# Kernel tuning notes

Hardware: AMD Instinct MI355X
Metric: run time of the kernel (lower is better)

The kernel has to match this reference:

```python
import jax, jax.numpy as jnp
import numpy as np

H = 768
L = 9
M = 5            # max_span_length
CTX_RATIO = 0.5
NEG_INF = -1e30


def setup_inputs() -> dict:
    key = jax.random.key(0)
    ks = jax.random.split(key, 12)
    B, S = 4, 2048
    sc = 1.0 / np.sqrt(H)
    return {
        "sequence_output": jax.random.normal(ks[0], (B, S, H), dtype=jnp.float32),
        "Wc": jax.random.normal(ks[1], (H, L), dtype=jnp.float32) * sc,
        "bc": jnp.zeros((L,), dtype=jnp.float32),
        "wa": jax.random.normal(ks[2], (H,), dtype=jnp.float32) * sc,
        "ba": jnp.zeros((), dtype=jnp.float32),
        "W1": jax.random.normal(ks[3], (2 * H, H), dtype=jnp.float32) * (1.0 / np.sqrt(2 * H)),
        "b1": jnp.zeros((H,), dtype=jnp.float32),
        "gamma": jnp.ones((H,), dtype=jnp.float32),
        "beta": jnp.zeros((H,), dtype=jnp.float32),
        "W2": jax.random.normal(ks[4], (H, L), dtype=jnp.float32) * sc,
        "b2": jnp.zeros((L,), dtype=jnp.float32),
    }


def reference(sequence_output, Wc, bc, wa, ba, W1, b1, gamma, beta, W2, b2):
    x = sequence_output                        # [B,S,H]
    B, S, _ = x.shape
    base_logits = jnp.einsum('bsh,hl->bsl', x, Wc) + bc   # [B,S,L]

    # sliding-window indices: window [i-M, i+M] clipped to [0, S)
    offsets = jnp.arange(-M, M + 1)            # [W]
    idx = jnp.arange(S)[:, None] + offsets     # [S,W]
    valid = (idx >= 0) & (idx < S)             # [S,W]
    idx_c = jnp.clip(idx, 0, S - 1)            # [S,W]

    # attention scores over window (span_attention linear -> scalar per token)
    scores = jnp.einsum('bsh,h->bs', x, wa) + ba           # [B,S]
    win_scores = scores[:, idx_c]                          # [B,S,W]
    win_scores = jnp.where(valid[None], win_scores, NEG_INF)
    attn = jax.nn.softmax(win_scores, axis=-1)             # [B,S,W]

    win_tokens = x[:, idx_c]                               # [B,S,W,H] gather
    weighted_ctx = jnp.einsum('bsw,bswh->bsh', attn, win_tokens)

    token_with_ctx = jnp.concatenate([x, weighted_ctx], axis=-1)  # [B,S,2H]
    h = jnp.einsum('bsd,dh->bsh', token_with_ctx, W1) + b1
    # LayerNorm (eps = 1e-5, torch default)
    mu = jnp.mean(h, axis=-1, keepdims=True)
    var = jnp.mean((h - mu) ** 2, axis=-1, keepdims=True)
    h = (h - mu) * jax.lax.rsqrt(var + 1e-5) * gamma + beta
    h = jax.nn.gelu(h, approximate=False)                  # torch nn.GELU default (erf)
    ctx_logits = jnp.einsum('bsh,hl->bsl', h, W2) + b2

    return (1.0 - CTX_RATIO) * base_logits + CTX_RATIO * ctx_logits
```

## Files before the change

### kernel.cpp

```cpp
#include <hip/hip_runtime.h>
#include <hip/hip_bf16.h>
#include <math.h>

#define S_LEN 2048
#define BATCH 4
#define HDIM 768
#define LOUT 9
#define NROWS (BATCH*S_LEN)
#define K2H 1536
#define KHALF 768
#define WIN 11
#define NEG_INF_F (-1e30f)

typedef __attribute__((ext_vector_type(4))) float f32x4;
typedef __attribute__((ext_vector_type(8))) short bf16x8;

static __device__ __forceinline__ void async_ld16(const void* g, void* l) {
  __builtin_amdgcn_global_load_lds((const __attribute__((address_space(1))) void*)g,
                                   (__attribute__((address_space(3))) void*)l, 16, 0, 0);
}

static __device__ __forceinline__ unsigned short f2bf(float f) {
  union { float f; unsigned int u; } v; v.f = f;
  unsigned int u = v.u;
  unsigned int r = (u + 0x7fffu + ((u >> 16) & 1u)) >> 16;
  return (unsigned short)r;
}

static __device__ __forceinline__ float bf2f(unsigned short h) {
  union { unsigned int u; float f; } v; v.u = ((unsigned int)h) << 16;
  return v.f;
}

__global__ __launch_bounds__(256) void k_prep(const float* __restrict__ W1,
                                              unsigned short* __restrict__ W1t,
                                              const float* __restrict__ x,
                                              const float* __restrict__ wa,
                                              const float* __restrict__ ba,
                                              const float* __restrict__ Wc,
                                              const float* __restrict__ bc,
                                              unsigned short* __restrict__ xc,
                                              float* __restrict__ scores,
                                              float* __restrict__ base) {
  __shared__ float tile[32][33];
  if (blockIdx.x < 1152) {
    int bk = blockIdx.x % 48;
    int bn = blockIdx.x / 48;
    int tc = threadIdx.x % 32;
    int tr = threadIdx.x / 32;
    #pragma unroll
    for (int i = 0; i < 32; i += 8) {
      tile[tr + i][tc] = W1[(bk*32 + tr + i) * HDIM + bn*32 + tc];
    }
    __syncthreads();
    #pragma unroll
    for (int i = 0; i < 32; i += 8) {
      W1t[(bn*32 + tr + i) * K2H + bk*32 + tc] = f2bf(tile[tc][tr + i]);
    }
    return;
  }
  int bid = blockIdx.x - 1152;
  int lane = threadIdx.x & 63, wave = threadIdx.x >> 6;
  int row = bid * 4 + wave;
  const float* xr = x + (long)row * HDIM + lane * 12;
  float xv[12];
  { const float4 a = *(const float4*)(xr);
    const float4 b4 = *(const float4*)(xr + 4);
    const float4 c4 = *(const float4*)(xr + 8);
    xv[0]=a.x; xv[1]=a.y; xv[2]=a.z; xv[3]=a.w;
    xv[4]=b4.x; xv[5]=b4.y; xv[6]=b4.z; xv[7]=b4.w;
    xv[8]=c4.x; xv[9]=c4.y; xv[10]=c4.z; xv[11]=c4.w; }
  unsigned short* dst = xc + (long)row * K2H + lane * 12;
  #pragma unroll
  for (int q = 0; q < 3; ++q) {
    ushort4 o;
    o.x = f2bf(xv[q*4+0]); o.y = f2bf(xv[q*4+1]);
    o.z = f2bf(xv[q*4+2]); o.w = f2bf(xv[q*4+3]);
    *(ushort4*)(dst + q*4) = o;
  }
  const float* war = wa + lane * 12;
  float sc = 0.f;
  #pragma unroll
  for (int q = 0; q < 3; ++q) {
    const float4 w4 = *(const float4*)(war + q*4);
    sc += xv[q*4+0]*w4.x + xv[q*4+1]*w4.y + xv[q*4+2]*w4.z + xv[q*4+3]*w4.w;
  }
  const float* wcr = Wc + (long)lane * 12 * LOUT;
  float p[LOUT] = {};
  #pragma unroll
  for (int j = 0; j < 12; ++j) {
    const float xj = xv[j];
    #pragma unroll
    for (int l = 0; l < LOUT; ++l) p[l] += xj * wcr[j * LOUT + l];
  }
  #pragma unroll
  for (int m = 1; m < 64; m <<= 1) {
    sc += __shfl_xor(sc, m);
    #pragma unroll
    for (int l = 0; l < LOUT; ++l) p[l] += __shfl_xor(p[l], m);
  }
  if (lane == 0) {
    scores[row] = sc + ba[0];
    #pragma unroll
    for (int l = 0; l < LOUT; ++l) base[row * LOUT + l] = p[l] + bc[l];
  }
}

__global__ __launch_bounds__(256) void k_ctx(const float* __restrict__ scores,
                                             unsigned short* __restrict__ xc) {
  int lane = threadIdx.x & 63, wave = threadIdx.x >> 6;
  int row = blockIdx.x * 4 + wave;
  int b = row >> 11, s = row & 2047;
  float sw[WIN];
  int jcs[WIN];
  #pragma unroll
  for (int w = 0; w < WIN; ++w) {
    int j = s - 5 + w;
    bool valid = (j >= 0) && (j < S_LEN);
    int jc = valid ? j : (j < 0 ? 0 : S_LEN - 1);
    jcs[w] = b * S_LEN + jc;
    sw[w] = valid ? scores[b * S_LEN + jc] : NEG_INF_F;
  }
  float mx = sw[0];
  #pragma unroll
  for (int w = 1; w < WIN; ++w) mx = fmaxf(mx, sw[w]);
  float es[WIN], ssum = 0.f;
  #pragma unroll
  for (int w = 0; w < WIN; ++w) {
    es[w] = (sw[w] > -1e29f) ? __expf(sw[w] - mx) : 0.f;
    ssum += es[w];
  }
  float inv = 1.f / ssum;
  float c[12] = {};
  #pragma unroll
  for (int w = 0; w < WIN; ++w) {
    float aw = es[w] * inv;
    const unsigned short* src = xc + (long)jcs[w] * K2H + lane * 12;
    #pragma unroll
    for (int q = 0; q < 3; ++q) {
      const ushort4 uv = *(const ushort4*)(src + q*4);
      c[q*4+0] += aw * bf2f(uv.x);
      c[q*4+1] += aw * bf2f(uv.y);
      c[q*4+2] += aw * bf2f(uv.z);
      c[q*4+3] += aw * bf2f(uv.w);
    }
  }
  unsigned short* dst = xc + (long)row * K2H + HDIM + lane * 12;
  #pragma unroll
  for (int q = 0; q < 3; ++q) {
    ushort4 o;
    o.x = f2bf(c[q*4+0]); o.y = f2bf(c[q*4+1]);
    o.z = f2bf(c[q*4+2]); o.w = f2bf(c[q*4+3]);
    *(ushort4*)(dst + q*4) = o;
  }
}

__global__ __launch_bounds__(256, 3) void k_gemm(const unsigned short* __restrict__ A,
                                                 const unsigned short* __restrict__ Bt,
                                                 unsigned short* __restrict__ Hout) {
  __shared__ unsigned short As[2][128 * 32];
  __shared__ unsigned short Bs[2][128 * 32];
  int bid = blockIdx.x;
  int obid = (bid & 7) * 96 + (bid >> 3);
  int kh = obid / 384;
  int mt = obid % 384;
  int bm = mt / 6, bn = mt % 6;
  int t = threadIdx.x;
  int lane = t & 63, wave = t >> 6;
  int wm = wave >> 1, wn = wave & 1;

  int rowc = lane >> 2;
  int fST = ((lane >> 2) ^ (lane >> 4)) & 3;
  int sST = (lane & 3) ^ fST;
  const unsigned short* gA0 = A  + (long)(bm * 128 + wave * 16 + rowc) * K2H + kh * KHALF + sST * 8;
  const unsigned short* gB0 = Bt + (long)(bn * 128 + wave * 16 + rowc) * K2H + kh * KHALF + sST * 8;

  int fR = ((lane & 3) ^ ((lane >> 2) & 3)) & 3;
  int slR = ((lane >> 4) ^ fR) & 3;
  int arow = wm * 64 + (lane & 15);
  int brow = wn * 64 + (lane & 15);

  f32x4 acc[4][4] = {};

#define STAGE(buf, kt) do {                                                    \
    async_ld16(gA0 + (kt),            &As[buf][(wave * 16) * 32]);             \
    async_ld16(gA0 + 64 * K2H + (kt), &As[buf][(64 + wave * 16) * 32]);        \
    async_ld16(gB0 + (kt),            &Bs[buf][(wave * 16) * 32]);             \
    async_ld16(gB0 + 64 * K2H + (kt), &Bs[buf][(64 + wave * 16) * 32]);        \
  } while (0)

#define COMPUTE(buf) do {                                                      \
    bf16x8 af[4], bfv[4];                                                      \
    _Pragma("unroll")                                                          \
    for (int m = 0; m < 4; ++m)                                                \
      af[m] = *(const bf16x8*)(&As[buf][(arow + m * 16) * 32 + slR * 8]);      \
    _Pragma("unroll")                                                          \
    for (int n = 0; n < 4; ++n)                                                \
      bfv[n] = *(const bf16x8*)(&Bs[buf][(brow + n * 16) * 32 + slR * 8]);     \
    _Pragma("unroll")                                                          \
    for (int m = 0; m < 4; ++m)                                                \
      _Pragma("unroll")                                                        \
      for (int n = 0; n < 4; ++n)                                              \
        acc[m][n] = __builtin_amdgcn_mfma_f32_16x16x32_bf16(af[m], bfv[n], acc[m][n], 0, 0, 0); \
  } while (0)

  STAGE(0, 0);
  __syncthreads();
  int cur = 0;
  #pragma unroll 1
  for (int tt = 0; tt < 23; ++tt) {
    STAGE(cur ^ 1, (tt + 1) * 32);
    COMPUTE(cur);
    __syncthreads();
    cur ^= 1;
  }
  COMPUTE(cur);

  unsigned short* Hp = Hout + (long)kh * NROWS * HDIM;
  int orow = bm * 128 + wm * 64 + (lane >> 4) * 4;
  int ocol = bn * 128 + wn * 64 + (lane & 15);
  #pragma unroll
  for (int m = 0; m < 4; ++m)
    #pragma unroll
    for (int n = 0; n < 4; ++n) {
      int col = ocol + n * 16;
      #pragma unroll
      for (int r = 0; r < 4; ++r) {
        Hp[(long)(orow + m * 16 + r) * HDIM + col] = f2bf(acc[m][n][r]);
      }
    }
#undef STAGE
#undef COMPUTE
}

__global__ __launch_bounds__(256) void k_ln(const unsigned short* __restrict__ H0,
                                            const unsigned short* __restrict__ H1,
                                            const float* __restrict__ b1,
                                            const float* __restrict__ gamma,
                                            const float* __restrict__ beta,
                                            const float* __restrict__ W2,
                                            const float* __restrict__ b2,
                                            const float* __restrict__ base,
                                            float* __restrict__ out) {
  int lane = threadIdx.x & 63, wave = threadIdx.x >> 6;
  int row = blockIdx.x * 4 + wave;
  const unsigned short* h0p = H0 + (long)row * HDIM + lane * 12;
  const unsigned short* h1p = H1 + (long)row * HDIM + lane * 12;
  const float* b1p = b1 + lane * 12;
  float vv[12];
  #pragma unroll
  for (int q = 0; q < 3; ++q) {
    const ushort4 a = *(const ushort4*)(h0p + q*4);
    const ushort4 b4 = *(const ushort4*)(h1p + q*4);
    const float4 bb = *(const float4*)(b1p + q*4);
    vv[q*4+0] = bf2f(a.x) + bf2f(b4.x) + bb.x;
    vv[q*4+1] = bf2f(a.y) + bf2f(b4.y) + bb.y;
    vv[q*4+2] = bf2f(a.z) + bf2f(b4.z) + bb.z;
    vv[q*4+3] = bf2f(a.w) + bf2f(b4.w) + bb.w;
  }
  float s1 = 0.f, s2 = 0.f;
  #pragma unroll
  for (int j = 0; j < 12; ++j) { s1 += vv[j]; s2 += vv[j] * vv[j]; }
  #pragma unroll
  for (int m = 1; m < 64; m <<= 1) { s1 += __shfl_xor(s1, m); s2 += __shfl_xor(s2, m); }
  float mu = s1 * (1.f / HDIM);
  float var = s2 * (1.f / HDIM) - mu * mu;
  float rstd = rsqrtf(var + 1e-5f);
  const float* gp = gamma + lane * 12;
  const float* bp = beta + lane * 12;
  const float* w2r = W2 + (long)lane * 12 * LOUT;
  float p[LOUT] = {};
  #pragma unroll
  for (int q = 0; q < 3; ++q) {
    const float4 g4 = *(const float4*)(gp + q*4);
    const float4 be4 = *(const float4*)(bp + q*4);
    const float gv[4] = { g4.x, g4.y, g4.z, g4.w };
    const float bvv[4] = { be4.x, be4.y, be4.z, be4.w };
    #pragma unroll
    for (int k = 0; k < 4; ++k) {
      int j = q*4 + k;
      float g = (vv[j] - mu) * rstd * gv[k] + bvv[k];
      float gg = 0.5f * g * (1.f + erff(g * 0.70710678118654752f));
      #pragma unroll
      for (int l = 0; l < LOUT; ++l) p[l] += gg * w2r[j * LOUT + l];
    }
  }
  #pragma unroll
  for (int m = 1; m < 64; m <<= 1)
    #pragma unroll
    for (int l = 0; l < LOUT; ++l) p[l] += __shfl_xor(p[l], m);
  if (lane == 0) {
    #pragma unroll
    for (int l = 0; l < LOUT; ++l) {
      out[row * LOUT + l] = 0.5f * base[row * LOUT + l] + 0.5f * (p[l] + b2[l]);
    }
  }
}

extern "C" void kernel_launch(void* const* d_in, const int* in_sizes, int n_in,
                              void* d_out, int out_size, void* d_ws, size_t ws_size,
                              hipStream_t stream) {
  const float* x     = (const float*)d_in[0];
  const float* Wc    = (const float*)d_in[1];
  const float* bc    = (const float*)d_in[2];
  const float* wa    = (const float*)d_in[3];
  const float* ba    = (const float*)d_in[4];
  const float* W1    = (const float*)d_in[5];
  const float* b1    = (const float*)d_in[6];
  const float* gamma = (const float*)d_in[7];
  const float* beta  = (const float*)d_in[8];
  const float* W2    = (const float*)d_in[9];
  const float* b2    = (const float*)d_in[10];
  float* out = (float*)d_out;

  char* ws = (char*)d_ws;
  unsigned short* xc   = (unsigned short*)(ws);
  unsigned short* w1t  = (unsigned short*)(ws + 25165824);
  float* scores        = (float*)(ws + 27525120);
  float* base          = (float*)(ws + 27557888);
  unsigned short* hbuf = (unsigned short*)(ws + 27852800);

  k_prep <<<dim3(1152 + 2048), dim3(256), 0, stream>>>(W1, w1t, x, wa, ba, Wc, bc,
                                                       xc, scores, base);
  k_ctx  <<<dim3(2048), dim3(256), 0, stream>>>(scores, xc);
  k_gemm <<<dim3(768),  dim3(256), 0, stream>>>(xc, w1t, hbuf);
  k_ln   <<<dim3(2048), dim3(256), 0, stream>>>(hbuf, hbuf + (long)NROWS * HDIM, b1,
                                                gamma, beta, W2, b2, base, out);
}
```

Baseline: 171.0 us.

## Fuse four kernels into one persistent kernel with grid barriers

Merges the prep, context, GEMM and LayerNorm kernels into one persistent kernel of 768 blocks. The stages are separated by atomic-counter grid barriers, and the counter is reset by a memset before each launch. The aim is to remove the launch overhead and the gaps between kernels. In exchange it depends on all 768 blocks being resident at once (3 per CU is assumed), otherwise the barrier deadlocks. The elementwise stages now loop over rows with fewer waves and lose some occupancy.

```diff
diff --git a/kernel.cpp b/kernel.cpp
--- a/kernel.cpp
+++ b/kernel.cpp
@@ -11,6 +11,8 @@
 #define KHALF 768
 #define WIN 11
 #define NEG_INF_F (-1e30f)
+#define NBLK 768
+#define NWAVE (NBLK*4)
 
 typedef __attribute__((ext_vector_type(4))) float f32x4;
 typedef __attribute__((ext_vector_type(8))) short bf16x8;
@@ -32,155 +34,170 @@
   return v.f;
 }
 
-__global__ __launch_bounds__(256) void k_prep(const float* __restrict__ W1,
-                                              unsigned short* __restrict__ W1t,
-                                              const float* __restrict__ x,
-                                              const float* __restrict__ wa,
-                                              const float* __restrict__ ba,
-                                              const float* __restrict__ Wc,
-                                              const float* __restrict__ bc,
-                                              unsigned short* __restrict__ xc,
-                                              float* __restrict__ scores,
-                                              float* __restrict__ base) {
+static __device__ __forceinline__ void gridbar(unsigned* cnt, unsigned k) {
+  __syncthreads();
+  if (threadIdx.x == 0) {
+    __threadfence();
+    atomicAdd(cnt, 1u);
+    while (atomicAdd(cnt, 0u) < NBLK * k) __builtin_amdgcn_s_sleep(4);
+    __threadfence();
+  }
+  __syncthreads();
+}
+
+__global__ __launch_bounds__(256, 3)
+void k_fused(const float* __restrict__ x,
+             const float* __restrict__ Wc,
+             const float* __restrict__ bc,
+             const float* __restrict__ wa,
+             const float* __restrict__ ba,
+             const float* __restrict__ W1,
+             const float* __restrict__ b1,
+             const float* __restrict__ gamma,
+             const float* __restrict__ beta,
+             const float* __restrict__ W2,
+             const float* __restrict__ b2,
+             unsigned short* __restrict__ xc,
+             unsigned short* __restrict__ w1t,
+             float* __restrict__ scores,
+             float* __restrict__ base,
+             unsigned short* __restrict__ hbuf,
+             unsigned* __restrict__ barcnt,
+             float* __restrict__ out) {
   __shared__ float tile[32][33];
-  if (blockIdx.x < 1152) {
-    int bk = blockIdx.x % 48;
-    int bn = blockIdx.x / 48;
-    int tc = threadIdx.x % 32;
-    int tr = threadIdx.x / 32;
-    #pragma unroll
-    for (int i = 0; i < 32; i += 8) {
-      tile[tr + i][tc] = W1[(bk*32 + tr + i) * HDIM + bn*32 + tc];
-    }
-    __syncthreads();
-    #pragma unroll
-    for (int i = 0; i < 32; i += 8) {
-      W1t[(bn*32 + tr + i) * K2H + bk*32 + tc] = f2bf(tile[tc][tr + i]);
-    }
-    return;
-  }
-  int bid = blockIdx.x - 1152;
-  int lane = threadIdx.x & 63, wave = threadIdx.x >> 6;
-  int row = bid * 4 + wave;
-  const float* xr = x + (long)row * HDIM + lane * 12;
-  float xv[12];
-  { const float4 a = *(const float4*)(xr);
-    const float4 b4 = *(const float4*)(xr + 4);
-    const float4 c4 = *(const float4*)(xr + 8);
-    xv[0]=a.x; xv[1]=a.y; xv[2]=a.z; xv[3]=a.w;
-    xv[4]=b4.x; xv[5]=b4.y; xv[6]=b4.z; xv[7]=b4.w;
-    xv[8]=c4.x; xv[9]=c4.y; xv[10]=c4.z; xv[11]=c4.w; }
-  unsigned short* dst = xc + (long)row * K2H + lane * 12;
-  #pragma unroll
-  for (int q = 0; q < 3; ++q) {
-    ushort4 o;
-    o.x = f2bf(xv[q*4+0]); o.y = f2bf(xv[q*4+1]);
-    o.z = f2bf(xv[q*4+2]); o.w = f2bf(xv[q*4+3]);
-    *(ushort4*)(dst + q*4) = o;
-  }
-  const float* war = wa + lane * 12;
-  float sc = 0.f;
-  #pragma unroll
-  for (int q = 0; q < 3; ++q) {
-    const float4 w4 = *(const float4*)(war + q*4);
-    sc += xv[q*4+0]*w4.x + xv[q*4+1]*w4.y + xv[q*4+2]*w4.z + xv[q*4+3]*w4.w;
-  }
-  const float* wcr = Wc + (long)lane * 12 * LOUT;
-  float p[LOUT] = {};
-  #pragma unroll
-  for (int j = 0; j < 12; ++j) {
-    const float xj = xv[j];
-    #pragma unroll
-    for (int l = 0; l < LOUT; ++l) p[l] += xj * wcr[j * LOUT + l];
-  }
-  #pragma unroll
-  for (int m = 1; m < 64; m <<= 1) {
-    sc += __shfl_xor(sc, m);
-    #pragma unroll
-    for (int l = 0; l < LOUT; ++l) p[l] += __shfl_xor(p[l], m);
-  }
-  if (lane == 0) {
-    scores[row] = sc + ba[0];
-    #pragma unroll
-    for (int l = 0; l < LOUT; ++l) base[row * LOUT + l] = p[l] + bc[l];
-  }
-}
-
-__global__ __launch_bounds__(256) void k_ctx(const float* __restrict__ scores,
-                                             unsigned short* __restrict__ xc) {
-  int lane = threadIdx.x & 63, wave = threadIdx.x >> 6;
-  int row = blockIdx.x * 4 + wave;
-  int b = row >> 11, s = row & 2047;
-  float sw[WIN];
-  int jcs[WIN];
-  #pragma unroll
-  for (int w = 0; w < WIN; ++w) {
-    int j = s - 5 + w;
-    bool valid = (j >= 0) && (j < S_LEN);
-    int jc = valid ? j : (j < 0 ? 0 : S_LEN - 1);
-    jcs[w] = b * S_LEN + jc;
-    sw[w] = valid ? scores[b * S_LEN + jc] : NEG_INF_F;
-  }
-  float mx = sw[0];
-  #pragma unroll
-  for (int w = 1; w < WIN; ++w) mx = fmaxf(mx, sw[w]);
-  float es[WIN], ssum = 0.f;
-  #pragma unroll
-  for (int w = 0; w < WIN; ++w) {
-    es[w] = (sw[w] > -1e29f) ? __expf(sw[w] - mx) : 0.f;
-    ssum += es[w];
-  }
-  float inv = 1.f / ssum;
-  float c[12] = {};
-  #pragma unroll
-  for (int w = 0; w < WIN; ++w) {
-    float aw = es[w] * inv;
-    const unsigned short* src = xc + (long)jcs[w] * K2H + lane * 12;
-    #pragma unroll
-    for (int q = 0; q < 3; ++q) {
-      const ushort4 uv = *(const ushort4*)(src + q*4);
-      c[q*4+0] += aw * bf2f(uv.x);
-      c[q*4+1] += aw * bf2f(uv.y);
-      c[q*4+2] += aw * bf2f(uv.z);
-      c[q*4+3] += aw * bf2f(uv.w);
-    }
-  }
-  unsigned short* dst = xc + (long)row * K2H + HDIM + lane * 12;
-  #pragma unroll
-  for (int q = 0; q < 3; ++q) {
-    ushort4 o;
-    o.x = f2bf(c[q*4+0]); o.y = f2bf(c[q*4+1]);
-    o.z = f2bf(c[q*4+2]); o.w = f2bf(c[q*4+3]);
-    *(ushort4*)(dst + q*4) = o;
-  }
-}
-
-__global__ __launch_bounds__(256, 3) void k_gemm(const unsigned short* __restrict__ A,
-                                                 const unsigned short* __restrict__ Bt,
-                                                 unsigned short* __restrict__ Hout) {
   __shared__ unsigned short As[2][128 * 32];
   __shared__ unsigned short Bs[2][128 * 32];
-  int bid = blockIdx.x;
-  int obid = (bid & 7) * 96 + (bid >> 3);
-  int kh = obid / 384;
-  int mt = obid % 384;
-  int bm = mt / 6, bn = mt % 6;
-  int t = threadIdx.x;
-  int lane = t & 63, wave = t >> 6;
-  int wm = wave >> 1, wn = wave & 1;
-
-  int rowc = lane >> 2;
-  int fST = ((lane >> 2) ^ (lane >> 4)) & 3;
-  int sST = (lane & 3) ^ fST;
-  const unsigned short* gA0 = A  + (long)(bm * 128 + wave * 16 + rowc) * K2H + kh * KHALF + sST * 8;
-  const unsigned short* gB0 = Bt + (long)(bn * 128 + wave * 16 + rowc) * K2H + kh * KHALF + sST * 8;
-
-  int fR = ((lane & 3) ^ ((lane >> 2) & 3)) & 3;
-  int slR = ((lane >> 4) ^ fR) & 3;
-  int arow = wm * 64 + (lane & 15);
-  int brow = wn * 64 + (lane & 15);
-
-  f32x4 acc[4][4] = {};
+  int lane = threadIdx.x & 63, wave = threadIdx.x >> 6;
+  int gwid = blockIdx.x * 4 + wave;
+
+  for (int j = blockIdx.x; j < 1152; j += NBLK) {
+    int bk = j % 48, bn = j / 48;
+    int tc = threadIdx.x % 32, tr = threadIdx.x / 32;
+    #pragma unroll
+    for (int i = 0; i < 32; i += 8)
+      tile[tr + i][tc] = W1[(bk*32 + tr + i) * HDIM + bn*32 + tc];
+    __syncthreads();
+    #pragma unroll
+    for (int i = 0; i < 32; i += 8)
+      w1t[(bn*32 + tr + i) * K2H + bk*32 + tc] = f2bf(tile[tc][tr + i]);
+    __syncthreads();
+  }
+
+  for (int row = gwid; row < NROWS; row += NWAVE) {
+    const float* xr = x + (long)row * HDIM + lane * 12;
+    float xv[12];
+    { const float4 a = *(const float4*)(xr);
+      const float4 b4 = *(const float4*)(xr + 4);
+      const float4 c4 = *(const float4*)(xr + 8);
+      xv[0]=a.x; xv[1]=a.y; xv[2]=a.z; xv[3]=a.w;
+      xv[4]=b4.x; xv[5]=b4.y; xv[6]=b4.z; xv[7]=b4.w;
+      xv[8]=c4.x; xv[9]=c4.y; xv[10]=c4.z; xv[11]=c4.w; }
+    unsigned short* dst = xc + (long)row * K2H + lane * 12;
+    #pragma unroll
+    for (int q = 0; q < 3; ++q) {
+      ushort4 o;
+      o.x = f2bf(xv[q*4+0]); o.y = f2bf(xv[q*4+1]);
+      o.z = f2bf(xv[q*4+2]); o.w = f2bf(xv[q*4+3]);
+      *(ushort4*)(dst + q*4) = o;
+    }
+    const float* war = wa + lane * 12;
+    float sc = 0.f;
+    #pragma unroll
+    for (int q = 0; q < 3; ++q) {
+      const float4 w4 = *(const float4*)(war + q*4);
+      sc += xv[q*4+0]*w4.x + xv[q*4+1]*w4.y + xv[q*4+2]*w4.z + xv[q*4+3]*w4.w;
+    }
+    const float* wcr = Wc + (long)lane * 12 * LOUT;
+    float p[LOUT] = {};
+    #pragma unroll
+    for (int j = 0; j < 12; ++j) {
+      const float xj = xv[j];
+      #pragma unroll
+      for (int l = 0; l < LOUT; ++l) p[l] += xj * wcr[j * LOUT + l];
+    }
+    #pragma unroll
+    for (int m = 1; m < 64; m <<= 1) {
+      sc += __shfl_xor(sc, m);
+      #pragma unroll
+      for (int l = 0; l < LOUT; ++l) p[l] += __shfl_xor(p[l], m);
+    }
+    if (lane == 0) {
+      scores[row] = sc + ba[0];
+      #pragma unroll
+      for (int l = 0; l < LOUT; ++l) base[row * LOUT + l] = p[l] + bc[l];
+    }
+  }
+
+  gridbar(barcnt, 1);
+
+  for (int row = gwid; row < NROWS; row += NWAVE) {
+    int b = row >> 11, s = row & 2047;
+    float sw[WIN];
+    int jcs[WIN];
+    #pragma unroll
+    for (int w = 0; w < WIN; ++w) {
+      int j = s - 5 + w;
+      bool valid = (j >= 0) && (j < S_LEN);
+      int jc = valid ? j : (j < 0 ? 0 : S_LEN - 1);
+      jcs[w] = b * S_LEN + jc;
+      sw[w] = valid ? scores[b * S_LEN + jc] : NEG_INF_F;
+    }
+    float mx = sw[0];
+    #pragma unroll
+    for (int w = 1; w < WIN; ++w) mx = fmaxf(mx, sw[w]);
+    float es[WIN], ssum = 0.f;
+    #pragma unroll
+    for (int w = 0; w < WIN; ++w) {
+      es[w] = (sw[w] > -1e29f) ? __expf(sw[w] - mx) : 0.f;
+      ssum += es[w];
+    }
+    float inv = 1.f / ssum;
+    float c[12] = {};
+    #pragma unroll
+    for (int w = 0; w < WIN; ++w) {
+      float aw = es[w] * inv;
+      const unsigned short* src = xc + (long)jcs[w] * K2H + lane * 12;
+      #pragma unroll
+      for (int q = 0; q < 3; ++q) {
+        const ushort4 uv = *(const ushort4*)(src + q*4);
+        c[q*4+0] += aw * bf2f(uv.x);
+        c[q*4+1] += aw * bf2f(uv.y);
+        c[q*4+2] += aw * bf2f(uv.z);
+        c[q*4+3] += aw * bf2f(uv.w);
+      }
+    }
+    unsigned short* dst = xc + (long)row * K2H + HDIM + lane * 12;
+    #pragma unroll
+    for (int q = 0; q < 3; ++q) {
+      ushort4 o;
+      o.x = f2bf(c[q*4+0]); o.y = f2bf(c[q*4+1]);
+      o.z = f2bf(c[q*4+2]); o.w = f2bf(c[q*4+3]);
+      *(ushort4*)(dst + q*4) = o;
+    }
+  }
+
+  gridbar(barcnt, 2);
+
+  {
+    int bid = blockIdx.x;
+    int obid = (bid & 7) * 96 + (bid >> 3);
+    int kh = obid / 384;
+    int mt = obid % 384;
+    int bm = mt / 6, bn = mt % 6;
+    int wm = wave >> 1, wn = wave & 1;
+
+    int rowc = lane >> 2;
+    int fST = ((lane >> 2) ^ (lane >> 4)) & 3;
+    int sST = (lane & 3) ^ fST;
+    const unsigned short* gA0 = xc  + (long)(bm * 128 + wave * 16 + rowc) * K2H + kh * KHALF + sST * 8;
+    const unsigned short* gB0 = w1t + (long)(bn * 128 + wave * 16 + rowc) * K2H + kh * KHALF + sST * 8;
+
+    int fR = ((lane & 3) ^ ((lane >> 2) & 3)) & 3;
+    int slR = ((lane >> 4) ^ fR) & 3;
+    int arow = wm * 64 + (lane & 15);
+    int brow = wn * 64 + (lane & 15);
+
+    f32x4 acc[4][4] = {};
 
 #define STAGE(buf, kt) do {                                                    \
     async_ld16(gA0 + (kt),            &As[buf][(wave * 16) * 32]);             \
@@ -204,95 +221,90 @@
         acc[m][n] = __builtin_amdgcn_mfma_f32_16x16x32_bf16(af[m], bfv[n], acc[m][n], 0, 0, 0); \
   } while (0)
 
-  STAGE(0, 0);
-  __syncthreads();
-  int cur = 0;
-  #pragma unroll 1
-  for (int tt = 0; tt < 23; ++tt) {
-    STAGE(cur ^ 1, (tt + 1) * 32);
+    STAGE(0, 0);
+    __syncthreads();
+    int cur = 0;
+    #pragma unroll 1
+    for (int tt = 0; tt < 23; ++tt) {
+      STAGE(cur ^ 1, (tt + 1) * 32);
+      COMPUTE(cur);
+      __syncthreads();
+      cur ^= 1;
+    }
     COMPUTE(cur);
-    __syncthreads();
-    cur ^= 1;
-  }
-  COMPUTE(cur);
-
-  unsigned short* Hp = Hout + (long)kh * NROWS * HDIM;
-  int orow = bm * 128 + wm * 64 + (lane >> 4) * 4;
-  int ocol = bn * 128 + wn * 64 + (lane & 15);
-  #pragma unroll
-  for (int m = 0; m < 4; ++m)
-    #pragma unroll
-    for (int n = 0; n < 4; ++n) {
-      int col = ocol + n * 16;
-      #pragma unroll
-      for (int r = 0; r < 4; ++r) {
-        Hp[(long)(orow + m * 16 + r) * HDIM + col] = f2bf(acc[m][n][r]);
+
+    unsigned short* Hp = hbuf + (long)kh * NROWS * HDIM;
+    int orow = bm * 128 + wm * 64 + (lane >> 4) * 4;
+    int ocol = bn * 128 + wn * 64 + (lane & 15);
+    #pragma unroll
+    for (int m = 0; m < 4; ++m)
+      #pragma unroll
+      for (int n = 0; n < 4; ++n) {
+        int col = ocol + n * 16;
+        #pragma unroll
+        for (int r = 0; r < 4; ++r) {
+          Hp[(long)(orow + m * 16 + r) * HDIM + col] = f2bf(acc[m][n][r]);
+        }
       }
-    }
 #undef STAGE
 #undef COMPUTE
-}
-
-__global__ __launch_bounds__(256) void k_ln(const unsigned short* __restrict__ H0,
-                                            const unsigned short* __restrict__ H1,
-                                            const float* __restrict__ b1,
-                                            const float* __restrict__ gamma,
-                                            const float* __restrict__ beta,
-                                            const float* __restrict__ W2,
-                                            const float* __restrict__ b2,
-                                            const float* __restrict__ base,
-                                            float* __restrict__ out) {
-  int lane = threadIdx.x & 63, wave = threadIdx.x >> 6;
-  int row = blockIdx.x * 4 + wave;
-  const unsigned short* h0p = H0 + (long)row * HDIM + lane * 12;
-  const unsigned short* h1p = H1 + (long)row * HDIM + lane * 12;
-  const float* b1p = b1 + lane * 12;
-  float vv[12];
-  #pragma unroll
-  for (int q = 0; q < 3; ++q) {
-    const ushort4 a = *(const ushort4*)(h0p + q*4);
-    const ushort4 b4 = *(const ushort4*)(h1p + q*4);
-    const float4 bb = *(const float4*)(b1p + q*4);
-    vv[q*4+0] = bf2f(a.x) + bf2f(b4.x) + bb.x;
-    vv[q*4+1] = bf2f(a.y) + bf2f(b4.y) + bb.y;
-    vv[q*4+2] = bf2f(a.z) + bf2f(b4.z) + bb.z;
-    vv[q*4+3] = bf2f(a.w) + bf2f(b4.w) + bb.w;
-  }
-  float s1 = 0.f, s2 = 0.f;
-  #pragma unroll
-  for (int j = 0; j < 12; ++j) { s1 += vv[j]; s2 += vv[j] * vv[j]; }
-  #pragma unroll
-  for (int m = 1; m < 64; m <<= 1) { s1 += __shfl_xor(s1, m); s2 += __shfl_xor(s2, m); }
-  float mu = s1 * (1.f / HDIM);
-  float var = s2 * (1.f / HDIM) - mu * mu;
-  float rstd = rsqrtf(var + 1e-5f);
-  const float* gp = gamma + lane * 12;
-  const float* bp = beta + lane * 12;
-  const float* w2r = W2 + (long)lane * 12 * LOUT;
-  float p[LOUT] = {};
-  #pragma unroll
-  for (int q = 0; q < 3; ++q) {
-    const float4 g4 = *(const float4*)(gp + q*4);
-    const float4 be4 = *(const float4*)(bp + q*4);
-    const float gv[4] = { g4.x, g4.y, g4.z, g4.w };
-    const float bvv[4] = { be4.x, be4.y, be4.z, be4.w };
-    #pragma unroll
-    for (int k = 0; k < 4; ++k) {
-      int j = q*4 + k;
-      float g = (vv[j] - mu) * rstd * gv[k] + bvv[k];
-      float gg = 0.5f * g * (1.f + erff(g * 0.70710678118654752f));
-      #pragma unroll
-      for (int l = 0; l < LOUT; ++l) p[l] += gg * w2r[j * LOUT + l];
-    }
-  }
-  #pragma unroll
-  for (int m = 1; m < 64; m <<= 1)
-    #pragma unroll
-    for (int l = 0; l < LOUT; ++l) p[l] += __shfl_xor(p[l], m);
-  if (lane == 0) {
-    #pragma unroll
-    for (int l = 0; l < LOUT; ++l) {
-      out[row * LOUT + l] = 0.5f * base[row * LOUT + l] + 0.5f * (p[l] + b2[l]);
+  }
+
+  gridbar(barcnt, 3);
+
+  const unsigned short* H0 = hbuf;
+  const unsigned short* H1 = hbuf + (long)NROWS * HDIM;
+  for (int row = gwid; row < NROWS; row += NWAVE) {
+    const unsigned short* h0p = H0 + (long)row * HDIM + lane * 12;
+    const unsigned short* h1p = H1 + (long)row * HDIM + lane * 12;
+    const float* b1p = b1 + lane * 12;
+    float vv[12];
+    #pragma unroll
+    for (int q = 0; q < 3; ++q) {
+      const ushort4 a = *(const ushort4*)(h0p + q*4);
+      const ushort4 b4 = *(const ushort4*)(h1p + q*4);
+      const float4 bb = *(const float4*)(b1p + q*4);
+      vv[q*4+0] = bf2f(a.x) + bf2f(b4.x) + bb.x;
+      vv[q*4+1] = bf2f(a.y) + bf2f(b4.y) + bb.y;
+      vv[q*4+2] = bf2f(a.z) + bf2f(b4.z) + bb.z;
+      vv[q*4+3] = bf2f(a.w) + bf2f(b4.w) + bb.w;
+    }
+    float s1 = 0.f, s2 = 0.f;
+    #pragma unroll
+    for (int j = 0; j < 12; ++j) { s1 += vv[j]; s2 += vv[j] * vv[j]; }
+    #pragma unroll
+    for (int m = 1; m < 64; m <<= 1) { s1 += __shfl_xor(s1, m); s2 += __shfl_xor(s2, m); }
+    float mu = s1 * (1.f / HDIM);
+    float var = s2 * (1.f / HDIM) - mu * mu;
+    float rstd = rsqrtf(var + 1e-5f);
+    const float* gp = gamma + lane * 12;
+    const float* bp = beta + lane * 12;
+    const float* w2r = W2 + (long)lane * 12 * LOUT;
+    float p[LOUT] = {};
+    #pragma unroll
+    for (int q = 0; q < 3; ++q) {
+      const float4 g4 = *(const float4*)(gp + q*4);
+      const float4 be4 = *(const float4*)(bp + q*4);
+      const float gv[4] = { g4.x, g4.y, g4.z, g4.w };
+      const float bvv[4] = { be4.x, be4.y, be4.z, be4.w };
+      #pragma unroll
+      for (int k2 = 0; k2 < 4; ++k2) {
+        int j = q*4 + k2;
+        float g = (vv[j] - mu) * rstd * gv[k2] + bvv[k2];
+        float gg = 0.5f * g * (1.f + erff(g * 0.70710678118654752f));
+        #pragma unroll
+        for (int l = 0; l < LOUT; ++l) p[l] += gg * w2r[j * LOUT + l];
+      }
+    }
+    #pragma unroll
+    for (int m = 1; m < 64; m <<= 1)
+      #pragma unroll
+      for (int l = 0; l < LOUT; ++l) p[l] += __shfl_xor(p[l], m);
+    if (lane == 0) {
+      #pragma unroll
+      for (int l = 0; l < LOUT; ++l) {
+        out[row * LOUT + l] = 0.5f * base[row * LOUT + l] + 0.5f * (p[l] + b2[l]);
+      }
     }
   }
 }
@@ -319,11 +331,11 @@
   float* scores        = (float*)(ws + 27525120);
   float* base          = (float*)(ws + 27557888);
   unsigned short* hbuf = (unsigned short*)(ws + 27852800);
-
-  k_prep <<<dim3(1152 + 2048), dim3(256), 0, stream>>>(W1, w1t, x, wa, ba, Wc, bc,
-                                                       xc, scores, base);
-  k_ctx  <<<dim3(2048), dim3(256), 0, stream>>>(scores, xc);
-  k_gemm <<<dim3(768),  dim3(256), 0, stream>>>(xc, w1t, hbuf);
-  k_ln   <<<dim3(2048), dim3(256), 0, stream>>>(hbuf, hbuf + (long)NROWS * HDIM, b1,
-                                                gamma, beta, W2, b2, base, out);
-}
+  unsigned* barcnt     = (unsigned*)(ws + 53018624);
+
+  hipMemsetAsync(barcnt, 0, 128, stream);
+  k_fused<<<dim3(NBLK), dim3(256), 0, stream>>>(x, Wc, bc, wa, ba, W1, b1,
+                                                gamma, beta, W2, b2,
+                                                xc, w1t, scores, base, hbuf,
+                                                barcnt, out);
+}
```

After: 476.0 us. 2.78x slower.
